# Kernel optimization log

Hardware: AMD Instinct MI355X
Metric: run time of the kernel (lower is better)

Reference implementation:

```python
import jax, jax.numpy as jnp
import numpy as np

D_MODEL = 768
N_HEADS = 12
HEAD_DIM = D_MODEL // N_HEADS


def setup_inputs() -> dict:
    key = jax.random.key(0)
    ks = jax.random.split(key, 9)
    s = 1.0 / np.sqrt(D_MODEL)
    inp = {
        "inputs": jax.random.normal(ks[0], (1, 4096, D_MODEL), dtype=jnp.float32),
        "Wq": jax.random.uniform(ks[1], (D_MODEL, D_MODEL), jnp.float32, -s, s),
        "bq": jax.random.uniform(ks[2], (D_MODEL,), jnp.float32, -s, s),
        "Wk": jax.random.uniform(ks[3], (D_MODEL, D_MODEL), jnp.float32, -s, s),
        "bk": jax.random.uniform(ks[4], (D_MODEL,), jnp.float32, -s, s),
        "Wv": jax.random.uniform(ks[5], (D_MODEL, D_MODEL), jnp.float32, -s, s),
        "bv": jax.random.uniform(ks[6], (D_MODEL,), jnp.float32, -s, s),
        "Wo": jax.random.uniform(ks[7], (D_MODEL, D_MODEL), jnp.float32, -s, s),
        "bo": jax.random.uniform(ks[8], (D_MODEL,), jnp.float32, -s, s),
    }
    return inp


def reference(inputs, Wq, bq, Wk, bk, Wv, bv, Wo, bo):
    B, S, D = inputs.shape
    H, Hd = N_HEADS, HEAD_DIM

    def split_heads(x):  # [B,S,D] -> [B,H,S,Hd]
        return x.reshape(B, S, H, Hd).transpose(0, 2, 1, 3)

    # nn.Linear computes x @ W.T + b
    Q = split_heads(inputs @ Wq.T + bq)
    K = split_heads(inputs @ Wk.T + bk)
    V = split_heads(inputs @ Wv.T + bv)

    scores = jnp.einsum("bhsd,bhtd->bhst", Q, K) / jnp.sqrt(jnp.float32(Hd))
    causal = jnp.tril(jnp.ones((S, S), dtype=bool))  # True = keep
    scores = jnp.where(causal, scores, -jnp.inf)
    attn = jax.nn.softmax(scores, axis=-1)  # dropout is identity in eval

    out = jnp.einsum("bhst,bhtd->bhsd", attn, V)
    out = out.transpose(0, 2, 1, 3).reshape(B, S, D)
    return out @ Wo.T + bo
```

## Files before the change

kernel.cpp:

```cpp
#include <hip/hip_runtime.h>
#include <stdint.h>

#define SEQ 4096
#define DM 768
#define NH 12
#define HD 64

typedef unsigned short u16;
typedef short short8 __attribute__((ext_vector_type(8)));
typedef float floatx4 __attribute__((ext_vector_type(4)));
typedef u16 u16x4 __attribute__((ext_vector_type(4)));

__device__ inline u16 f2b(float f) {
  union { float f; uint32_t u; } v; v.f = f;
  uint32_t u = v.u;
  return (u16)((u + 0x7fffu + ((u >> 16) & 1u)) >> 16);
}

__device__ inline float b2f(u16 x) {
  union { uint32_t u; float f; } v; v.u = ((uint32_t)x) << 16;
  return v.f;
}

#if defined(__has_builtin)
#if __has_builtin(__builtin_amdgcn_cvt_pk_bf16_f32)
#define HAVE_PK_BF16 1
#endif
#endif

__device__ inline uint32_t pk_bf16(float a, float b) {
#ifdef HAVE_PK_BF16
  typedef __bf16 bf16x2_t __attribute__((ext_vector_type(2)));
  union { bf16x2_t v; uint32_t u; } c;
  c.v = __builtin_amdgcn_cvt_pk_bf16_f32(a, b);
  return c.u;
#else
  return (uint32_t)f2b(a) | ((uint32_t)f2b(b) << 16);
#endif
}

__device__ inline void load_lds16(const void* g, void* l) {
  __builtin_amdgcn_global_load_lds(
      (const __attribute__((address_space(1))) uint32_t*)g,
      (__attribute__((address_space(3))) uint32_t*)l, 16, 0, 0);
}

__global__ __launch_bounds__(256) void convert_all(
    const float* __restrict__ X, const float* __restrict__ Wq,
    const float* __restrict__ Wk, const float* __restrict__ Wv,
    const float* __restrict__ Wo,
    u16* __restrict__ Xb, u16* __restrict__ Wqb, u16* __restrict__ Wkb,
    u16* __restrict__ Wvb, u16* __restrict__ Wob) {
  int t = blockIdx.x * 256 + threadIdx.x;
  const int NX = SEQ * DM / 4;
  const int NW = DM * DM / 4;
  const float* src; u16* dst; int off;
  if (t < NX)               { src = X;  dst = Xb;  off = t; }
  else if (t < NX + NW)     { src = Wq; dst = Wqb; off = t - NX; }
  else if (t < NX + 2 * NW) { src = Wk; dst = Wkb; off = t - NX - NW; }
  else if (t < NX + 3 * NW) { src = Wv; dst = Wvb; off = t - NX - 2 * NW; }
  else if (t < NX + 4 * NW) { src = Wo; dst = Wob; off = t - NX - 3 * NW; }
  else return;
  float4 v = *(const float4*)(src + (size_t)off * 4);
  uint2 o;
  o.x = pk_bf16(v.x, v.y);
  o.y = pk_bf16(v.z, v.w);
  *(uint2*)(dst + (size_t)off * 4) = o;
}

__global__ __launch_bounds__(256) void gemm_qkv(
    const u16* __restrict__ Xb,
    const u16* __restrict__ Wqb, const u16* __restrict__ Wkb,
    const u16* __restrict__ Wvb,
    const float* __restrict__ bq, const float* __restrict__ bk,
    const float* __restrict__ bv,
    u16* __restrict__ Qh, u16* __restrict__ Kh, u16* __restrict__ VtG) {
  const u16* W; const float* bias;
  const int z = blockIdx.z;
  if (z == 0)      { W = Wqb; bias = bq; }
  else if (z == 1) { W = Wkb; bias = bk; }
  else             { W = Wvb; bias = bv; }

  __shared__ u16 smem[32768];

  const int tid = threadIdx.x;
  const int wave = tid >> 6, lane = tid & 63;
  const int g = lane >> 4, ln = lane & 15;
  const int m0 = blockIdx.y * 128, n0 = blockIdx.x * 128;
  const int wm = (wave & 1) * 64, wn = (wave >> 1) * 64;
  const int srow = lane >> 3;
  const int schunk = (lane & 7) ^ srow;
  const int swz = ln & 7;

  floatx4 acc[4][4] = {};

#pragma unroll
  for (int i = 0; i < 4; ++i) {
    int u = wave * 4 + i;
    load_lds16(Xb + (size_t)(m0 + u * 8 + srow) * DM + schunk * 8, smem + u * 512);
    load_lds16(W + (size_t)(n0 + u * 8 + srow) * DM + schunk * 8,
               smem + 16384 + u * 512);
  }

  for (int kt = 0; kt < 12; ++kt) {
    const int cur = kt & 1;
    __syncthreads();
    if (kt < 11) {
      const int k0 = (kt + 1) * 64, nb = cur ^ 1;
#pragma unroll
      for (int i = 0; i < 4; ++i) {
        int u = wave * 4 + i;
        load_lds16(Xb + (size_t)(m0 + u * 8 + srow) * DM + k0 + schunk * 8,
                   smem + nb * 8192 + u * 512);
        load_lds16(W + (size_t)(n0 + u * 8 + srow) * DM + k0 + schunk * 8,
                   smem + 16384 + nb * 8192 + u * 512);
      }
    }
    const u16* Ac = smem + cur * 8192;
    const u16* Bc = smem + 16384 + cur * 8192;
    short8 af[4][2], bf[4][2];
#pragma unroll
    for (int mi = 0; mi < 4; ++mi)
#pragma unroll
      for (int kh = 0; kh < 2; ++kh)
        af[mi][kh] = *(const short8*)(Ac + (wm + mi * 16 + ln) * 64 +
                                      ((kh * 4 + g) ^ swz) * 8);
#pragma unroll
    for (int ni = 0; ni < 4; ++ni)
#pragma unroll
      for (int kh = 0; kh < 2; ++kh)
        bf[ni][kh] = *(const short8*)(Bc + (wn + ni * 16 + ln) * 64 +
                                      ((kh * 4 + g) ^ swz) * 8);
#pragma unroll
    for (int kh = 0; kh < 2; ++kh)
#pragma unroll
      for (int mi = 0; mi < 4; ++mi)
#pragma unroll
        for (int ni = 0; ni < 4; ++ni)
          acc[mi][ni] = __builtin_amdgcn_mfma_f32_16x16x32_bf16(
              af[mi][kh], bf[ni][kh], acc[mi][ni], 0, 0, 0);
  }

  const float qscale = 0.125f * 1.44269504089f;
  __syncthreads();

  if (z == 2) {
#pragma unroll
    for (int mi = 0; mi < 4; ++mi) {
      int row0 = wm + mi * 16 + g * 4;
#pragma unroll
      for (int ni = 0; ni < 4; ++ni) {
        int col = wn + ni * 16 + ln;
        float b = bias[n0 + col];
        uint2 o;
        o.x = pk_bf16(acc[mi][ni][0] + b, acc[mi][ni][1] + b);
        o.y = pk_bf16(acc[mi][ni][2] + b, acc[mi][ni][3] + b);
        *(uint2*)(smem + col * 136 + row0) = o;
      }
    }
    __syncthreads();
#pragma unroll
    for (int t = 0; t < 8; ++t) {
      int unit = tid + t * 256;
      int dcol = unit >> 4, ch = unit & 15;
      short8 v = *(const short8*)(smem + dcol * 136 + ch * 8);
      int col = n0 + dcol, hh = col >> 6, dd = col & 63;
      *(short8*)(VtG + ((size_t)(hh * 64 + dd)) * SEQ + m0 + ch * 8) = v;
    }
  } else {
    u16* out = (z == 0) ? Qh : Kh;
    float cs = (z == 0) ? qscale : 1.0f;
#pragma unroll
    for (int mi = 0; mi < 4; ++mi) {
      int row0 = wm + mi * 16 + g * 4;
#pragma unroll
      for (int ni = 0; ni < 4; ++ni) {
        int col = wn + ni * 16 + ln;
        float b = bias[n0 + col];
        uint32_t w0 = pk_bf16((acc[mi][ni][0] + b) * cs, (acc[mi][ni][1] + b) * cs);
        uint32_t w1 = pk_bf16((acc[mi][ni][2] + b) * cs, (acc[mi][ni][3] + b) * cs);
        smem[(row0 + 0) * 136 + col] = (u16)w0;
        smem[(row0 + 1) * 136 + col] = (u16)(w0 >> 16);
        smem[(row0 + 2) * 136 + col] = (u16)w1;
        smem[(row0 + 3) * 136 + col] = (u16)(w1 >> 16);
      }
    }
    __syncthreads();
#pragma unroll
    for (int t = 0; t < 8; ++t) {
      int unit = tid + t * 256;
      int row = unit >> 4, ch = unit & 15;
      short8 v = *(const short8*)(smem + row * 136 + ch * 8);
      int col = n0 + ch * 8, hh = col >> 6, dd = col & 63;
      *(short8*)(out + ((size_t)hh * SEQ + m0 + row) * HD + dd) = v;
    }
  }
}

#define CHUNK 16
__global__ __launch_bounds__(512, 6) void attn_chunk(
    const u16* __restrict__ Qh, const u16* __restrict__ Kh,
    const u16* __restrict__ VtG, u16* __restrict__ Opart,
    float2* __restrict__ Mlp) {
  const int h = blockIdx.x;
  const int b = 79 - blockIdx.y;
  int qB, ci;
  if (b < 8)       { qB = b;               ci = 0; }
  else if (b < 24) { int r = b - 8;  qB = 8 + (r >> 1); ci = r & 1; }
  else if (b < 48) { int r = b - 24; int d = r / 3; qB = 16 + d; ci = r - d * 3; }
  else             { int r = b - 48; qB = 24 + (r >> 2); ci = r & 3; }
  const int kb0 = ci * CHUNK;
  const int kb1 = min(kb0 + CHUNK, 2 * qB + 2);

  const int tid = threadIdx.x, wave = tid >> 6, lane = tid & 63;
  const int g = lane >> 4, ln = lane & 15;
  const int q0 = qB * 128;
  const int qwave = q0 + wave * 16;
  const int srow = lane >> 3;
  const int schunk = (lane & 7) ^ srow;
  const int swz = ln & 7;

  __shared__ u16 Ks[2 * 4096];
  __shared__ u16 Vt[2 * 4096];
  __shared__ u16 Ps[8][16 * 72];

  const int qglob = qwave + ln;
  const u16* Qbase = Qh + ((size_t)h * SEQ + qglob) * HD;
  short8 aq[2] = { *(const short8*)(Qbase + g * 8),
                   *(const short8*)(Qbase + 32 + g * 8) };

  floatx4 oacc[4] = {};
  float m_i = -1e30f, l_i = 0.f;
  u16* PsW = &Ps[wave][0];

  const size_t kbase = (size_t)h * SEQ * HD;
  const size_t vbase = (size_t)h * 64 * SEQ;

  load_lds16(Kh + kbase + (size_t)(kb0 * 64 + wave * 8 + srow) * HD + schunk * 8,
             Ks + wave * 512);
  load_lds16(VtG + vbase + (size_t)(wave * 8 + srow) * SEQ + kb0 * 64 + schunk * 8,
             Vt + wave * 512);

  for (int kb = kb0; kb < kb1; ++kb) {
    const int cur = (kb - kb0) & 1;
    __syncthreads();
    if (kb + 1 < kb1) {
      const int nb = cur ^ 1, kn = (kb + 1) * 64;
      load_lds16(Kh + kbase + (size_t)(kn + wave * 8 + srow) * HD + schunk * 8,
                 Ks + nb * 4096 + wave * 512);
      load_lds16(VtG + vbase + (size_t)(wave * 8 + srow) * SEQ + kn + schunk * 8,
                 Vt + nb * 4096 + wave * 512);
    }
    const u16* Kc = Ks + cur * 4096;
    const u16* Vc = Vt + cur * 4096;

    if (kb * 64 > qwave + 15) continue;

    floatx4 st[4] = {};
#pragma unroll
    for (int kh = 0; kh < 2; ++kh)
#pragma unroll
      for (int nt = 0; nt < 4; ++nt) {
        short8 kf = *(const short8*)(Kc + (nt * 16 + ln) * 64 +
                                     ((kh * 4 + g) ^ swz) * 8);
        st[nt] = __builtin_amdgcn_mfma_f32_16x16x32_bf16(kf, aq[kh], st[nt], 0, 0, 0);
      }

    if (kb * 64 + 63 > qwave) {
#pragma unroll
      for (int nt = 0; nt < 4; ++nt)
#pragma unroll
        for (int r = 0; r < 4; ++r)
          if (kb * 64 + nt * 16 + g * 4 + r > qglob) st[nt][r] = -1e30f;
    }

    float mx = -1e30f;
#pragma unroll
    for (int nt = 0; nt < 4; ++nt)
#pragma unroll
      for (int r = 0; r < 4; ++r) mx = fmaxf(mx, st[nt][r]);
    mx = fmaxf(mx, __shfl_xor(mx, 16));
    mx = fmaxf(mx, __shfl_xor(mx, 32));
    float mnew = fmaxf(m_i, mx);
    float alpha = __builtin_amdgcn_exp2f(m_i - mnew);
    m_i = mnew;
    float rs = 0.f;
#pragma unroll
    for (int nt = 0; nt < 4; ++nt)
#pragma unroll
      for (int r = 0; r < 4; ++r) {
        float e = __builtin_amdgcn_exp2f(st[nt][r] - mnew);
        st[nt][r] = e;
        rs += e;
      }
    rs += __shfl_xor(rs, 16);
    rs += __shfl_xor(rs, 32);
    l_i = l_i * alpha + rs;
#pragma unroll
    for (int nt = 0; nt < 4; ++nt) oacc[nt] *= alpha;

#pragma unroll
    for (int nt = 0; nt < 4; ++nt) {
      uint2 pk;
      pk.x = pk_bf16(st[nt][0], st[nt][1]);
      pk.y = pk_bf16(st[nt][2], st[nt][3]);
      *(uint2*)(PsW + ln * 72 + nt * 16 + g * 4) = pk;
    }

#pragma unroll
    for (int ks = 0; ks < 2; ++ks) {
      short8 ap = *(const short8*)(PsW + ln * 72 + ks * 32 + g * 8);
#pragma unroll
      for (int nt = 0; nt < 4; ++nt) {
        short8 vf = *(const short8*)(Vc + (nt * 16 + ln) * 64 +
                                     ((ks * 4 + g) ^ swz) * 8);
        oacc[nt] = __builtin_amdgcn_mfma_f32_16x16x32_bf16(vf, ap, oacc[nt], 0, 0, 0);
      }
    }
  }

  const int slot = (h * 32 + qB) * 4 + ci;
  float inv = 1.f / l_i;
  int qloc = wave * 16 + ln;
  u16* Op = Opart + (size_t)slot * 8192 + qloc * 64;
#pragma unroll
  for (int nt = 0; nt < 4; ++nt) {
    uint2 o;
    o.x = pk_bf16(oacc[nt][0] * inv, oacc[nt][1] * inv);
    o.y = pk_bf16(oacc[nt][2] * inv, oacc[nt][3] * inv);
    *(uint2*)(Op + nt * 16 + g * 4) = o;
  }
  if (g == 0) Mlp[(size_t)slot * 128 + qloc] = make_float2(m_i, l_i);
}

__global__ __launch_bounds__(256) void attn_merge(
    const u16* __restrict__ Opart, const float2* __restrict__ Mlp,
    u16* __restrict__ Ob) {
  const int h = blockIdx.x, qB = blockIdx.y;
  const int n = (qB >> 3) + 1;
  const int base = (h * 32 + qB) * 4;
  const int q = threadIdx.x >> 1;
  const int d0 = (threadIdx.x & 1) * 32;

  float m[4], l[4];
  float M = -1e30f;
  for (int i = 0; i < n; ++i) {
    float2 ml = Mlp[(size_t)(base + i) * 128 + q];
    m[i] = ml.x; l[i] = ml.y;
    M = fmaxf(M, m[i]);
  }
  float w[4], L = 0.f;
  for (int i = 0; i < n; ++i) {
    w[i] = l[i] * __builtin_amdgcn_exp2f(m[i] - M);
    L += w[i];
  }
  float invL = 1.f / L;

  float acc[32];
#pragma unroll
  for (int j = 0; j < 32; ++j) acc[j] = 0.f;
  for (int i = 0; i < n; ++i) {
    float wi = w[i] * invL;
    const u16* src = Opart + (size_t)(base + i) * 8192 + q * 64 + d0;
#pragma unroll
    for (int c = 0; c < 4; ++c) {
      short8 a = ((const short8*)src)[c];
#pragma unroll
      for (int j = 0; j < 8; ++j) acc[c * 8 + j] += wi * b2f((u16)a[j]);
    }
  }

  u16* dst = Ob + (size_t)(qB * 128 + q) * DM + h * HD + d0;
#pragma unroll
  for (int c = 0; c < 4; ++c) {
    uint4 o;
    o.x = pk_bf16(acc[c * 8 + 0], acc[c * 8 + 1]);
    o.y = pk_bf16(acc[c * 8 + 2], acc[c * 8 + 3]);
    o.z = pk_bf16(acc[c * 8 + 4], acc[c * 8 + 5]);
    o.w = pk_bf16(acc[c * 8 + 6], acc[c * 8 + 7]);
    ((uint4*)dst)[c] = o;
  }
}

__global__ __launch_bounds__(256) void gemm_out(
    const u16* __restrict__ Ab, const u16* __restrict__ Wob,
    const float* __restrict__ bo, float* __restrict__ Cout) {
  __shared__ u16 smem[16384];

  const int tid = threadIdx.x;
  const int wave = tid >> 6, lane = tid & 63;
  const int g = lane >> 4, ln = lane & 15;
  const int m0 = blockIdx.y * 64, n0 = blockIdx.x * 64;
  const int wm = (wave & 1) * 32, wn = (wave >> 1) * 32;
  const int srow = lane >> 3;
  const int schunk = (lane & 7) ^ srow;
  const int swz = ln & 7;

  floatx4 acc[2][2] = {};

#pragma unroll
  for (int i = 0; i < 2; ++i) {
    int u = wave * 2 + i;
    load_lds16(Ab + (size_t)(m0 + u * 8 + srow) * DM + schunk * 8, smem + u * 512);
    load_lds16(Wob + (size_t)(n0 + u * 8 + srow) * DM + schunk * 8,
               smem + 8192 + u * 512);
  }

  for (int kt = 0; kt < 12; ++kt) {
    const int cur = kt & 1;
    __syncthreads();
    if (kt < 11) {
      const int k0 = (kt + 1) * 64, nb = cur ^ 1;
#pragma unroll
      for (int i = 0; i < 2; ++i) {
        int u = wave * 2 + i;
        load_lds16(Ab + (size_t)(m0 + u * 8 + srow) * DM + k0 + schunk * 8,
                   smem + nb * 4096 + u * 512);
        load_lds16(Wob + (size_t)(n0 + u * 8 + srow) * DM + k0 + schunk * 8,
                   smem + 8192 + nb * 4096 + u * 512);
      }
    }
    const u16* Ac = smem + cur * 4096;
    const u16* Bc = smem + 8192 + cur * 4096;
    short8 af[2][2], bf[2][2];
#pragma unroll
    for (int mi = 0; mi < 2; ++mi)
#pragma unroll
      for (int kh = 0; kh < 2; ++kh)
        af[mi][kh] = *(const short8*)(Ac + (wm + mi * 16 + ln) * 64 +
                                      ((kh * 4 + g) ^ swz) * 8);
#pragma unroll
    for (int ni = 0; ni < 2; ++ni)
#pragma unroll
      for (int kh = 0; kh < 2; ++kh)
        bf[ni][kh] = *(const short8*)(Bc + (wn + ni * 16 + ln) * 64 +
                                      ((kh * 4 + g) ^ swz) * 8);
#pragma unroll
    for (int kh = 0; kh < 2; ++kh)
#pragma unroll
      for (int mi = 0; mi < 2; ++mi)
#pragma unroll
        for (int ni = 0; ni < 2; ++ni)
          acc[mi][ni] = __builtin_amdgcn_mfma_f32_16x16x32_bf16(
              af[mi][kh], bf[ni][kh], acc[mi][ni], 0, 0, 0);
  }

#pragma unroll
  for (int mi = 0; mi < 2; ++mi) {
    int row = m0 + wm + mi * 16 + g * 4;
#pragma unroll
    for (int ni = 0; ni < 2; ++ni) {
      int col = n0 + wn + ni * 16 + ln;
      float b = bo[col];
#pragma unroll
      for (int r = 0; r < 4; ++r)
        Cout[(size_t)(row + r) * DM + col] = acc[mi][ni][r] + b;
    }
  }
}

extern "C" void kernel_launch(void* const* d_in, const int* in_sizes, int n_in,
                              void* d_out, int out_size, void* d_ws, size_t ws_size,
                              hipStream_t stream) {
  const float* X  = (const float*)d_in[0];
  const float* Wq = (const float*)d_in[1];
  const float* bq = (const float*)d_in[2];
  const float* Wk = (const float*)d_in[3];
  const float* bk = (const float*)d_in[4];
  const float* Wv = (const float*)d_in[5];
  const float* bv = (const float*)d_in[6];
  const float* Wo = (const float*)d_in[7];
  const float* bo = (const float*)d_in[8];
  float* out = (float*)d_out;

  char* ws = (char*)d_ws;
  u16* Xb  = (u16*)ws; ws += (size_t)SEQ * DM * 2;
  u16* Wqb = (u16*)ws; ws += (size_t)DM * DM * 2;
  u16* Wkb = (u16*)ws; ws += (size_t)DM * DM * 2;
  u16* Wvb = (u16*)ws; ws += (size_t)DM * DM * 2;
  u16* Wob = (u16*)ws; ws += (size_t)DM * DM * 2;
  u16* Qh  = (u16*)ws; ws += (size_t)NH * SEQ * HD * 2;
  u16* Kh  = (u16*)ws; ws += (size_t)NH * SEQ * HD * 2;
  u16* VtG = (u16*)ws; ws += (size_t)NH * SEQ * HD * 2;
  u16* Ob  = (u16*)ws; ws += (size_t)SEQ * DM * 2;
  u16* Opart = (u16*)ws; ws += (size_t)NH * 32 * 4 * 128 * 64 * 2;
  float2* Mlp = (float2*)ws; ws += (size_t)NH * 32 * 4 * 128 * sizeof(float2);

  convert_all<<<5376, 256, 0, stream>>>(X, Wq, Wk, Wv, Wo, Xb, Wqb, Wkb, Wvb, Wob);

  dim3 gq(DM / 128, SEQ / 128, 3);
  gemm_qkv<<<gq, 256, 0, stream>>>(Xb, Wqb, Wkb, Wvb, bq, bk, bv, Qh, Kh, VtG);

  dim3 ga(NH, 80);
  attn_chunk<<<ga, 512, 0, stream>>>(Qh, Kh, VtG, Opart, Mlp);

  dim3 gm(NH, 32);
  attn_merge<<<gm, 256, 0, stream>>>(Opart, Mlp, Ob);

  dim3 go(DM / 64, SEQ / 64);
  gemm_out<<<go, 256, 0, stream>>>(Ob, Wob, bo, out);
}
```

Before: 188.1 us.

## Process two 16-row query tiles per wave in attention, halving block size

Each wave now owns 32 query rows (two 16-row MFMA tiles) instead of 16, with 4 waves per block instead of 8. Every K and V fragment read from LDS is reused for two MFMAs, which cuts LDS read traffic per unit of work, and each wave issues two K/V tile loads per stage. The cost is higher register pressure (doubled accumulators and scores), fewer waves to hide latency, and coarser causal skipping at 32-row granularity.

```diff
diff --git a/kernel.cpp b/kernel.cpp
--- a/kernel.cpp
+++ b/kernel.cpp
@@ -198,7 +198,7 @@
 }
 
 #define CHUNK 16
-__global__ __launch_bounds__(512, 6) void attn_chunk(
+__global__ __launch_bounds__(256, 3) void attn_chunk(
     const u16* __restrict__ Qh, const u16* __restrict__ Kh,
     const u16* __restrict__ VtG, u16* __restrict__ Opart,
     float2* __restrict__ Mlp) {
@@ -215,122 +215,146 @@
   const int tid = threadIdx.x, wave = tid >> 6, lane = tid & 63;
   const int g = lane >> 4, ln = lane & 15;
   const int q0 = qB * 128;
-  const int qwave = q0 + wave * 16;
+  const int qwave = q0 + wave * 32;
   const int srow = lane >> 3;
   const int schunk = (lane & 7) ^ srow;
   const int swz = ln & 7;
 
   __shared__ u16 Ks[2 * 4096];
   __shared__ u16 Vt[2 * 4096];
-  __shared__ u16 Ps[8][16 * 72];
-
-  const int qglob = qwave + ln;
-  const u16* Qbase = Qh + ((size_t)h * SEQ + qglob) * HD;
-  short8 aq[2] = { *(const short8*)(Qbase + g * 8),
-                   *(const short8*)(Qbase + 32 + g * 8) };
-
-  floatx4 oacc[4] = {};
-  float m_i = -1e30f, l_i = 0.f;
+  __shared__ u16 Ps[4][32 * 72];
+
+  short8 aq[2][2];
+#pragma unroll
+  for (int qs = 0; qs < 2; ++qs) {
+    const u16* Qbase = Qh + ((size_t)h * SEQ + qwave + qs * 16 + ln) * HD;
+    aq[qs][0] = *(const short8*)(Qbase + g * 8);
+    aq[qs][1] = *(const short8*)(Qbase + 32 + g * 8);
+  }
+
+  floatx4 oacc[2][4] = {};
+  float m_i[2] = {-1e30f, -1e30f}, l_i[2] = {0.f, 0.f};
   u16* PsW = &Ps[wave][0];
 
   const size_t kbase = (size_t)h * SEQ * HD;
   const size_t vbase = (size_t)h * 64 * SEQ;
 
-  load_lds16(Kh + kbase + (size_t)(kb0 * 64 + wave * 8 + srow) * HD + schunk * 8,
-             Ks + wave * 512);
-  load_lds16(VtG + vbase + (size_t)(wave * 8 + srow) * SEQ + kb0 * 64 + schunk * 8,
-             Vt + wave * 512);
+#pragma unroll
+  for (int i = 0; i < 2; ++i) {
+    int u = wave * 2 + i;
+    load_lds16(Kh + kbase + (size_t)(kb0 * 64 + u * 8 + srow) * HD + schunk * 8,
+               Ks + u * 512);
+    load_lds16(VtG + vbase + (size_t)(u * 8 + srow) * SEQ + kb0 * 64 + schunk * 8,
+               Vt + u * 512);
+  }
 
   for (int kb = kb0; kb < kb1; ++kb) {
     const int cur = (kb - kb0) & 1;
     __syncthreads();
     if (kb + 1 < kb1) {
       const int nb = cur ^ 1, kn = (kb + 1) * 64;
-      load_lds16(Kh + kbase + (size_t)(kn + wave * 8 + srow) * HD + schunk * 8,
-                 Ks + nb * 4096 + wave * 512);
-      load_lds16(VtG + vbase + (size_t)(wave * 8 + srow) * SEQ + kn + schunk * 8,
-                 Vt + nb * 4096 + wave * 512);
+#pragma unroll
+      for (int i = 0; i < 2; ++i) {
+        int u = wave * 2 + i;
+        load_lds16(Kh + kbase + (size_t)(kn + u * 8 + srow) * HD + schunk * 8,
+                   Ks + nb * 4096 + u * 512);
+        load_lds16(VtG + vbase + (size_t)(u * 8 + srow) * SEQ + kn + schunk * 8,
+                   Vt + nb * 4096 + u * 512);
+      }
     }
     const u16* Kc = Ks + cur * 4096;
     const u16* Vc = Vt + cur * 4096;
 
-    if (kb * 64 > qwave + 15) continue;
-
-    floatx4 st[4] = {};
+    if (kb * 64 > qwave + 31) continue;
+
+    floatx4 st[2][4] = {};
 #pragma unroll
     for (int kh = 0; kh < 2; ++kh)
 #pragma unroll
       for (int nt = 0; nt < 4; ++nt) {
         short8 kf = *(const short8*)(Kc + (nt * 16 + ln) * 64 +
                                      ((kh * 4 + g) ^ swz) * 8);
-        st[nt] = __builtin_amdgcn_mfma_f32_16x16x32_bf16(kf, aq[kh], st[nt], 0, 0, 0);
+        st[0][nt] = __builtin_amdgcn_mfma_f32_16x16x32_bf16(kf, aq[0][kh], st[0][nt], 0, 0, 0);
+        st[1][nt] = __builtin_amdgcn_mfma_f32_16x16x32_bf16(kf, aq[1][kh], st[1][nt], 0, 0, 0);
       }
 
     if (kb * 64 + 63 > qwave) {
 #pragma unroll
+      for (int qs = 0; qs < 2; ++qs) {
+        int qglob = qwave + qs * 16 + ln;
+#pragma unroll
+        for (int nt = 0; nt < 4; ++nt)
+#pragma unroll
+          for (int r = 0; r < 4; ++r)
+            if (kb * 64 + nt * 16 + g * 4 + r > qglob) st[qs][nt][r] = -1e30f;
+      }
+    }
+
+#pragma unroll
+    for (int qs = 0; qs < 2; ++qs) {
+      float mx = -1e30f;
+#pragma unroll
       for (int nt = 0; nt < 4; ++nt)
 #pragma unroll
-        for (int r = 0; r < 4; ++r)
-          if (kb * 64 + nt * 16 + g * 4 + r > qglob) st[nt][r] = -1e30f;
-    }
-
-    float mx = -1e30f;
-#pragma unroll
-    for (int nt = 0; nt < 4; ++nt)
-#pragma unroll
-      for (int r = 0; r < 4; ++r) mx = fmaxf(mx, st[nt][r]);
-    mx = fmaxf(mx, __shfl_xor(mx, 16));
-    mx = fmaxf(mx, __shfl_xor(mx, 32));
-    float mnew = fmaxf(m_i, mx);
-    float alpha = __builtin_amdgcn_exp2f(m_i - mnew);
-    m_i = mnew;
-    float rs = 0.f;
-#pragma unroll
-    for (int nt = 0; nt < 4; ++nt)
-#pragma unroll
-      for (int r = 0; r < 4; ++r) {
-        float e = __builtin_amdgcn_exp2f(st[nt][r] - mnew);
-        st[nt][r] = e;
-        rs += e;
-      }
-    rs += __shfl_xor(rs, 16);
-    rs += __shfl_xor(rs, 32);
-    l_i = l_i * alpha + rs;
-#pragma unroll
-    for (int nt = 0; nt < 4; ++nt) oacc[nt] *= alpha;
-
-#pragma unroll
-    for (int nt = 0; nt < 4; ++nt) {
-      uint2 pk;
-      pk.x = pk_bf16(st[nt][0], st[nt][1]);
-      pk.y = pk_bf16(st[nt][2], st[nt][3]);
-      *(uint2*)(PsW + ln * 72 + nt * 16 + g * 4) = pk;
+        for (int r = 0; r < 4; ++r) mx = fmaxf(mx, st[qs][nt][r]);
+      mx = fmaxf(mx, __shfl_xor(mx, 16));
+      mx = fmaxf(mx, __shfl_xor(mx, 32));
+      float mnew = fmaxf(m_i[qs], mx);
+      float alpha = __builtin_amdgcn_exp2f(m_i[qs] - mnew);
+      m_i[qs] = mnew;
+      float rs = 0.f;
+#pragma unroll
+      for (int nt = 0; nt < 4; ++nt)
+#pragma unroll
+        for (int r = 0; r < 4; ++r) {
+          float e = __builtin_amdgcn_exp2f(st[qs][nt][r] - mnew);
+          st[qs][nt][r] = e;
+          rs += e;
+        }
+      rs += __shfl_xor(rs, 16);
+      rs += __shfl_xor(rs, 32);
+      l_i[qs] = l_i[qs] * alpha + rs;
+#pragma unroll
+      for (int nt = 0; nt < 4; ++nt) oacc[qs][nt] *= alpha;
+
+#pragma unroll
+      for (int nt = 0; nt < 4; ++nt) {
+        uint2 pk;
+        pk.x = pk_bf16(st[qs][nt][0], st[qs][nt][1]);
+        pk.y = pk_bf16(st[qs][nt][2], st[qs][nt][3]);
+        *(uint2*)(PsW + (qs * 16 + ln) * 72 + nt * 16 + g * 4) = pk;
+      }
     }
 
 #pragma unroll
     for (int ks = 0; ks < 2; ++ks) {
-      short8 ap = *(const short8*)(PsW + ln * 72 + ks * 32 + g * 8);
+      short8 ap0 = *(const short8*)(PsW + (0 * 16 + ln) * 72 + ks * 32 + g * 8);
+      short8 ap1 = *(const short8*)(PsW + (1 * 16 + ln) * 72 + ks * 32 + g * 8);
 #pragma unroll
       for (int nt = 0; nt < 4; ++nt) {
         short8 vf = *(const short8*)(Vc + (nt * 16 + ln) * 64 +
                                      ((ks * 4 + g) ^ swz) * 8);
-        oacc[nt] = __builtin_amdgcn_mfma_f32_16x16x32_bf16(vf, ap, oacc[nt], 0, 0, 0);
+        oacc[0][nt] = __builtin_amdgcn_mfma_f32_16x16x32_bf16(vf, ap0, oacc[0][nt], 0, 0, 0);
+        oacc[1][nt] = __builtin_amdgcn_mfma_f32_16x16x32_bf16(vf, ap1, oacc[1][nt], 0, 0, 0);
       }
     }
   }
 
   const int slot = (h * 32 + qB) * 4 + ci;
-  float inv = 1.f / l_i;
-  int qloc = wave * 16 + ln;
-  u16* Op = Opart + (size_t)slot * 8192 + qloc * 64;
-#pragma unroll
-  for (int nt = 0; nt < 4; ++nt) {
-    uint2 o;
-    o.x = pk_bf16(oacc[nt][0] * inv, oacc[nt][1] * inv);
-    o.y = pk_bf16(oacc[nt][2] * inv, oacc[nt][3] * inv);
-    *(uint2*)(Op + nt * 16 + g * 4) = o;
-  }
-  if (g == 0) Mlp[(size_t)slot * 128 + qloc] = make_float2(m_i, l_i);
+#pragma unroll
+  for (int qs = 0; qs < 2; ++qs) {
+    float inv = 1.f / l_i[qs];
+    int qloc = wave * 32 + qs * 16 + ln;
+    u16* Op = Opart + (size_t)slot * 8192 + qloc * 64;
+#pragma unroll
+    for (int nt = 0; nt < 4; ++nt) {
+      uint2 o;
+      o.x = pk_bf16(oacc[qs][nt][0] * inv, oacc[qs][nt][1] * inv);
+      o.y = pk_bf16(oacc[qs][nt][2] * inv, oacc[qs][nt][3] * inv);
+      *(uint2*)(Op + nt * 16 + g * 4) = o;
+    }
+    if (g == 0) Mlp[(size_t)slot * 128 + qloc] = make_float2(m_i[qs], l_i[qs]);
+  }
 }
 
 __global__ __launch_bounds__(256) void attn_merge(
@@ -492,7 +516,7 @@
   gemm_qkv<<<gq, 256, 0, stream>>>(Xb, Wqb, Wkb, Wvb, bq, bk, bv, Qh, Kh, VtG);
 
   dim3 ga(NH, 80);
-  attn_chunk<<<ga, 512, 0, stream>>>(Qh, Kh, VtG, Opart, Mlp);
+  attn_chunk<<<ga, 256, 0, stream>>>(Qh, Kh, VtG, Opart, Mlp);
 
   dim3 gm(NH, 32);
   attn_merge<<<gm, 256, 0, stream>>>(Opart, Mlp, Ob);
```

Result: slower. 192.2 us (+2.2%).
